# Optimization experiments

Hardware: AMD Instinct MI355X
Metric: run time of the kernel (lower is better)

The kernel has to match this reference:

```python
import jax, jax.numpy as jnp
import numpy as np

NUM_CLASSES = 17
NUM_ENSEMBLE = 10
TAU = 10.0
TOP_K = 20  # min(self.k=20, filter_K=200)
EPS = 1e-12


def _l2norm(x, axis=-1):
    # matches F.normalize: x / max(||x||, 1e-12)
    n = jnp.sqrt(jnp.sum(x * x, axis=axis, keepdims=True))
    return x / jnp.maximum(n, EPS)


def _batch_ensemble(x, weight, alpha_be, gamma_be, ensemble_bias):
    # x: [M, D1] -> [E, M, D2]  (BatchEnsemble.forward, kept in [E, M, D2] layout)
    r = x[None, :, :] * alpha_be[:, None, :]              # [E, M, D1]
    w = jnp.einsum('emd,od->emo', r, weight)              # [E, M, D2]
    return w * gamma_be[:, None, :] + ensemble_bias[:, None, :]


def _compute_logits(z, supports, labels, weight, alpha_be, gamma_be, ensemble_bias):
    mlp_z = _batch_ensemble(z, weight, alpha_be, gamma_be, ensemble_bias)         # [E, B, D2]
    mlp_s = _batch_ensemble(supports, weight, alpha_be, gamma_be, ensemble_bias)  # [E, N, D2]
    lbl = labels / (jnp.sum(labels, axis=0, keepdims=True) + EPS)                 # [N, C]
    centroids = jnp.einsum('nc,end->ecd', lbl, mlp_s)                             # [E, C, D2]
    zn = _l2norm(mlp_z)
    cn = _l2norm(centroids)
    return TAU * jnp.einsum('ebd,ecd->ebc', zn, cn)                               # [E, B, C]


def _cosine_distance(X, Y):
    Xn = _l2norm(X, axis=1)
    Yn = _l2norm(Y, axis=1)
    XX = jnp.sum(Xn * Xn, axis=1)[:, None]   # [B, 1]
    YY = jnp.sum(Yn * Yn, axis=1)            # [N]
    XY = 2.0 * (Xn @ Yn.T)                   # [B, N]
    return XX + YY - XY


def _target_generation(z, supports, labels, weight, alpha_be, gamma_be, ensemble_bias):
    dist = _cosine_distance(z, supports)      # [B, N]
    W = jnp.exp(-dist)
    B = W.shape[0]
    _, idx = jax.lax.top_k(W, TOP_K)                                   # [B, K]
    mask = jnp.zeros_like(W).at[jnp.arange(B)[:, None], idx].set(1.0)  # [B, N]
    temp = _compute_logits(supports, supports, labels, weight, alpha_be, gamma_be, ensemble_bias)  # [E, N, C]
    tgt_oh = jax.nn.one_hot(jnp.argmax(temp, axis=-1), NUM_CLASSES, dtype=temp.dtype)  # [E, N, C]
    soft = jax.nn.softmax(temp, axis=-1)
    targets = jnp.einsum('bn,enc->ebc', mask, tgt_oh)
    targets = targets / (jnp.sum(targets, axis=2, keepdims=True) + EPS)
    outputs = jnp.einsum('bn,enc->ebc', mask, soft)
    outputs = outputs / (jnp.sum(outputs, axis=2, keepdims=True) + EPS)
    outputs = jnp.mean(outputs, axis=0)   # [B, C]
    return targets, outputs


def setup_inputs() -> dict:
    key = jax.random.key(0)
    ks = jax.random.split(key, 7)
    B, N, D1, D2, E, C = 4096, 3400, 2048, 1024, NUM_ENSEMBLE, NUM_CLASSES
    z = jax.random.normal(ks[0], (B, D1), dtype=jnp.float32)
    supports = jax.random.normal(ks[1], (N, D1), dtype=jnp.float32)
    y = jax.random.randint(ks[2], (N,), 0, C)
    labels = jax.nn.one_hot(y, C, dtype=jnp.float32)
    weight = jax.random.normal(ks[3], (D2, D1), dtype=jnp.float32) * 0.02
    alpha_be = 1.0 + 0.1 * jax.random.normal(ks[4], (E, D1), dtype=jnp.float32)
    gamma_be = 1.0 + 0.1 * jax.random.normal(ks[5], (E, D2), dtype=jnp.float32)
    ensemble_bias = jnp.zeros((E, D2), dtype=jnp.float32)
    return {"z": z, "supports": supports, "labels": labels, "weight": weight,
            "alpha_be": alpha_be, "gamma_be": gamma_be, "ensemble_bias": ensemble_bias}


def reference(z, supports, labels, weight, alpha_be, gamma_be, ensemble_bias):
    targets, outputs = _target_generation(z, supports, labels, weight, alpha_be, gamma_be, ensemble_bias)
    logits = _compute_logits(z, supports, labels, weight, alpha_be, gamma_be, ensemble_bias)  # [E, B, C]
    return outputs, logits
```

## Files before the change

### kernel.cpp

```cpp
#include <hip/hip_runtime.h>
#include <math.h>

#define B_    4096
#define N_    3400
#define NP2_  3584
#define D1_   2048
#define D2_   1024
#define E_    10
#define NE_   (E_ * D2_)
#define NDOT_ 256
#define NEX_  (NE_ + NDOT_)
#define ZOFF_ 3456
#define MR_   7680
#define EC_   170
#define C_    17
#define TOPK_ 20
#define CAND_ 24
#define TAU_  10.0f

typedef __bf16 bf16x8 __attribute__((ext_vector_type(8)));
typedef __bf16 bf16x4 __attribute__((ext_vector_type(4)));
typedef float  f32x4  __attribute__((ext_vector_type(4)));

#define MFMA_(a,b,c) __builtin_amdgcn_mfma_f32_16x16x32_bf16(a,b,c,0,0,0)

__device__ inline float wsum64(float v){
  #pragma unroll
  for (int m = 1; m < 64; m <<= 1) v += __shfl_xor(v, m);
  return v;
}

__device__ __forceinline__ void gload_lds16(const unsigned short* g, unsigned short* l){
  __builtin_amdgcn_global_load_lds(
      (const __attribute__((address_space(1))) void*)g,
      (__attribute__((address_space(3))) void*)l, 16, 0, 0);
}

__global__ __launch_bounds__(256)
void prep_rows(const float* __restrict__ X, unsigned short* __restrict__ hi,
               float* __restrict__ rinv){
  const int r = blockIdx.x, t = threadIdx.x;
  const float4* x4 = reinterpret_cast<const float4*>(X + (long)r * D1_);
  bf16x4* h4 = reinterpret_cast<bf16x4*>(hi + (long)r * D1_);
  float ss = 0.f;
  #pragma unroll
  for (int it = 0; it < 2; ++it){
    int i = t + it * 256;
    float4 v = x4[i];
    float f[4] = {v.x, v.y, v.z, v.w};
    bf16x4 h;
    #pragma unroll
    for (int j = 0; j < 4; ++j){
      ss += f[j] * f[j];
      h[j] = (__bf16)f[j];
    }
    h4[i] = h;
  }
  __shared__ float red[256];
  red[t] = ss; __syncthreads();
  for (int s = 128; s; s >>= 1){ if (t < s) red[t] += red[t + s]; __syncthreads(); }
  if (t == 0) rinv[r] = 1.f / fmaxf(sqrtf(red[0]), 1e-12f);
}

__global__ __launch_bounds__(256)
void zfill_all(uint4* p0, long n0, uint4* p1, long n1, uint4* p2, long n2,
               uint4* p3, long n3, uint4* p4, long n4){
  long i = (long)blockIdx.x * 256 + threadIdx.x;
  uint4 zz = make_uint4(0,0,0,0);
  if (i < n0){ p0[i] = zz; return; } i -= n0;
  if (i < n1){ p1[i] = zz; return; } i -= n1;
  if (i < n2){ p2[i] = zz; return; } i -= n2;
  if (i < n3){ p3[i] = zz; return; } i -= n3;
  if (i < n4){ p4[i] = zz; }
}

__global__ __launch_bounds__(256)
void labelprep(const float* __restrict__ labels, int* __restrict__ y, float* __restrict__ cnt){
  int n = blockIdx.x * 256 + threadIdx.x;
  if (n >= N_) return;
  int c = 0;
  #pragma unroll
  for (int cc = 0; cc < C_; ++cc) if (labels[n * C_ + cc] > 0.5f) c = cc;
  y[n] = c;
  atomicAdd(&cnt[c], 1.0f);
}

__global__ __launch_bounds__(256)
void wfold(const float* __restrict__ W, const float* __restrict__ alpha,
           unsigned short* __restrict__ wbf){
  long i = (long)blockIdx.x * 256 + threadIdx.x;
  const long perE = (long)D2_ * D1_ / 4;
  int e = (int)(i / perE);
  long r = i - (long)e * perE;
  int k4 = (int)(r & (D1_/4 - 1));
  float4 wv = reinterpret_cast<const float4*>(W)[r];
  float4 av = reinterpret_cast<const float4*>(alpha + (long)e * D1_)[k4];
  bf16x4 o;
  o[0] = (__bf16)(wv.x * av.x);
  o[1] = (__bf16)(wv.y * av.y);
  o[2] = (__bf16)(wv.z * av.z);
  o[3] = (__bf16)(wv.w * av.w);
  reinterpret_cast<bf16x4*>(wbf)[i] = o;
}

__global__ __launch_bounds__(256)
void transposeW(const float* __restrict__ W, float* __restrict__ WT){
  __shared__ float tile[32][33];
  const int bx = blockIdx.x, by = blockIdx.y;
  const int tx = threadIdx.x & 31, ty = threadIdx.x >> 5;
  #pragma unroll
  for (int i = 0; i < 4; ++i)
    tile[ty + i*8][tx] = W[(long)(by*32 + ty + i*8) * D1_ + bx*32 + tx];
  __syncthreads();
  #pragma unroll
  for (int i = 0; i < 4; ++i)
    WT[(long)(bx*32 + ty + i*8) * D2_ + by*32 + tx] = tile[tx][ty + i*8];
}

__global__ __launch_bounds__(256)
void pbuild(const float* __restrict__ S, const int* __restrict__ y,
            const float* __restrict__ cnt, float* __restrict__ part){
  __shared__ float acc[C_ * 256];
  __shared__ float winv[C_];
  const int t = threadIdx.x, kb = blockIdx.x * 256, s = blockIdx.y;
  #pragma unroll
  for (int c = 0; c < C_; ++c) acc[c * 256 + t] = 0.f;
  if (t < C_) winv[t] = 1.f / (cnt[t] + 1e-12f);
  __syncthreads();
  const int n0 = s * 425, n1 = n0 + 425;
  for (int n = n0; n < n1; ++n){
    int c = y[n];
    acc[c * 256 + t] += winv[c] * S[(long)n * D1_ + kb + t];
  }
  #pragma unroll
  for (int c = 0; c < C_; ++c)
    part[((long)s * C_ + c) * D1_ + kb + t] = acc[c * 256 + t];
}

__global__ __launch_bounds__(256)
void pa2(const float* __restrict__ part, const float* __restrict__ alpha,
         float* __restrict__ A2){
  int i = blockIdx.x * 256 + threadIdx.x;
  if (i >= EC_ * D1_) return;
  int ec = i >> 11, k = i & (D1_ - 1);
  int e = ec / C_, c = ec - e * C_;
  float s = 0.f;
  #pragma unroll
  for (int kz = 0; kz < 8; ++kz) s += part[((long)kz * C_ + c) * D1_ + k];
  A2[i] = s * alpha[(long)e * D1_ + k];
}

__global__ __launch_bounds__(256)
void redcent(const float* __restrict__ part2, const float* __restrict__ gamma,
             const float* __restrict__ bias, const float* __restrict__ cnt,
             float* __restrict__ cent){
  int i = blockIdx.x * 256 + threadIdx.x;
  if (i >= EC_ * D2_) return;
  int ec = i >> 10, d = i & (D2_ - 1);
  int e = ec / C_, c = ec - e * C_;
  float s = 0.f;
  #pragma unroll
  for (int kz = 0; kz < 8; ++kz) s += part2[(long)kz * EC_ * D2_ + i];
  float sc = cnt[c] / (cnt[c] + 1e-12f);
  cent[i] = gamma[(long)e * D2_ + d] * s + bias[(long)e * D2_ + d] * sc;
}

__global__ __launch_bounds__(256)
void normgcn(float* __restrict__ cent, const float* __restrict__ gamma,
             const float* __restrict__ bias, float* __restrict__ gcn,
             float* __restrict__ bconst){
  const int ec = blockIdx.x, t = threadIdx.x;
  const int e = ec / C_;
  float4* c4 = reinterpret_cast<float4*>(cent + (long)ec * D2_);
  float4 v = c4[t];
  float ss = v.x*v.x + v.y*v.y + v.z*v.z + v.w*v.w;
  __shared__ float red[256];
  red[t] = ss; __syncthreads();
  for (int s = 128; s; s >>= 1){ if (t < s) red[t] += red[t + s]; __syncthreads(); }
  float rinv = 1.f / fmaxf(sqrtf(red[0]), 1e-12f);
  v.x *= rinv; v.y *= rinv; v.z *= rinv; v.w *= rinv;
  c4[t] = v;
  float4 g = reinterpret_cast<const float4*>(gamma + (long)e * D2_)[t];
  reinterpret_cast<float4*>(gcn + (long)ec * D2_)[t] =
      make_float4(g.x*v.x, g.y*v.y, g.z*v.z, g.w*v.w);
  float4 bb = reinterpret_cast<const float4*>(bias + (long)e * D2_)[t];
  float bs = bb.x*v.x + bb.y*v.y + bb.z*v.z + bb.w*v.w;
  __syncthreads();
  red[t] = bs; __syncthreads();
  for (int s = 128; s; s >>= 1){ if (t < s) red[t] += red[t + s]; __syncthreads(); }
  if (t == 0) bconst[ec] = red[0];
}

__global__ __launch_bounds__(256)
void redgb(const float* __restrict__ part2, const float* __restrict__ alpha,
           unsigned short* __restrict__ wbf){
  int i = blockIdx.x * 256 + threadIdx.x;
  if (i >= EC_ * D1_) return;
  int ec = i >> 11, k = i & (D1_ - 1);
  int e = ec / C_;
  float s = 0.f;
  #pragma unroll
  for (int kz = 0; kz < 8; ++kz) s += part2[(long)kz * EC_ * D1_ + i];
  __bf16 b = (__bf16)(alpha[(long)e * D1_ + k] * s);
  wbf[(long)(NE_ + ec) * D1_ + k] = *(unsigned short*)&b;
}

__global__ __launch_bounds__(256)
void gemm64k(const float* __restrict__ A, int lda,
             const float* __restrict__ Bm, int ldb,
             float* __restrict__ part, int M, int N, int KC)
{
  __shared__ float As[16][68];
  __shared__ float Bs[16][68];
  const int kz = blockIdx.z;
  const int m0 = blockIdx.y * 64, n0 = blockIdx.x * 64;
  const int t  = threadIdx.x;
  const int lr = t >> 2;
  const int lk = (t & 3) << 2;
  const int ty4 = (t >> 4) << 2;
  const int tx4 = (t & 15) << 2;
  const bool aok = (m0 + lr) < M;
  const bool bok = (n0 + lr) < N;
  const float* ap = A  + (long)(m0 + lr) * lda + lk;
  const float* bp = Bm + (long)(n0 + lr) * ldb + lk;
  float acc[4][4] = {{0.f}};
  const int k0b = kz * KC, k0e = k0b + KC;
  for (int k0 = k0b; k0 < k0e; k0 += 16){
    float4 av = make_float4(0,0,0,0), bv = make_float4(0,0,0,0);
    if (aok) av = *reinterpret_cast<const float4*>(ap + k0);
    if (bok) bv = *reinterpret_cast<const float4*>(bp + k0);
    As[lk+0][lr] = av.x; As[lk+1][lr] = av.y; As[lk+2][lr] = av.z; As[lk+3][lr] = av.w;
    Bs[lk+0][lr] = bv.x; Bs[lk+1][lr] = bv.y; Bs[lk+2][lr] = bv.z; Bs[lk+3][lr] = bv.w;
    __syncthreads();
    #pragma unroll
    for (int kk = 0; kk < 16; ++kk){
      float4 a = *reinterpret_cast<const float4*>(&As[kk][ty4]);
      float4 b = *reinterpret_cast<const float4*>(&Bs[kk][tx4]);
      float aa[4] = {a.x, a.y, a.z, a.w};
      float bb[4] = {b.x, b.y, b.z, b.w};
      #pragma unroll
      for (int i = 0; i < 4; ++i)
        #pragma unroll
        for (int j = 0; j < 4; ++j)
          acc[i][j] += aa[i] * bb[j];
    }
    __syncthreads();
  }
  float* Out = part + (long)kz * M * N;
  #pragma unroll
  for (int i = 0; i < 4; ++i){
    int m = m0 + ty4 + i;
    if (m >= M) continue;
    #pragma unroll
    for (int j = 0; j < 4; ++j){
      int n = n0 + tx4 + j;
      if (n >= N) continue;
      Out[(long)m * N + n] = acc[i][j];
    }
  }
}

#define SA0(buf, kt) { gload_lds16(a0p+(kt)*64, &LA[buf][d00]); gload_lds16(a0p+(kt)*64+32, &LA[buf][d01]); }
#define SA1(buf, kt) { gload_lds16(a1p+(kt)*64, &LA[buf][d10]); gload_lds16(a1p+(kt)*64+32, &LA[buf][d11]); }
#define SB0(buf, kt) { gload_lds16(b0p+(kt)*64, &LB[buf][d00]); gload_lds16(b0p+(kt)*64+32, &LB[buf][d01]); }
#define SB1(buf, kt) { gload_lds16(b1p+(kt)*64, &LB[buf][d10]); gload_lds16(b1p+(kt)*64+32, &LB[buf][d11]); }

#define RD_A03(cb) { _Pragma("unroll") for (int i = 0; i < 4; ++i){ \
    ar[i][0] = *(const bf16x8*)&LA[cb][raB + (unsigned)(i*2  )*512]; \
    ar[i][1] = *(const bf16x8*)&LA[cb][raB + (unsigned)(i*2+1)*512]; } }
#define RD_A47(cb) { _Pragma("unroll") for (int i = 0; i < 4; ++i){ \
    ar[i][0] = *(const bf16x8*)&LA[cb][raB + (unsigned)((4+i)*2  )*512]; \
    ar[i][1] = *(const bf16x8*)&LA[cb][raB + (unsigned)((4+i)*2+1)*512]; } }
#define RD_B01(cb) { _Pragma("unroll") for (int j = 0; j < 2; ++j){ \
    brA[j][0] = *(const bf16x8*)&LB[cb][rbB + (unsigned)(j*2  )*512]; \
    brA[j][1] = *(const bf16x8*)&LB[cb][rbB + (unsigned)(j*2+1)*512]; } }
#define RD_B23(cb) { _Pragma("unroll") for (int j = 0; j < 2; ++j){ \
    brB[j][0] = *(const bf16x8*)&LB[cb][rbB + (unsigned)((2+j)*2  )*512]; \
    brB[j][1] = *(const bf16x8*)&LB[cb][rbB + (unsigned)((2+j)*2+1)*512]; } }

#define MM_Q0 { _Pragma("unroll") for (int ks = 0; ks < 2; ++ks) \
    _Pragma("unroll") for (int i = 0; i < 4; ++i) \
    _Pragma("unroll") for (int j = 0; j < 2; ++j) \
      acc[i][j] = MFMA_(ar[i][ks], brA[j][ks], acc[i][j]); }
#define MM_Q1 { _Pragma("unroll") for (int ks = 0; ks < 2; ++ks) \
    _Pragma("unroll") for (int i = 0; i < 4; ++i) \
    _Pragma("unroll") for (int j = 0; j < 2; ++j) \
      acc[i][2+j] = MFMA_(ar[i][ks], brB[j][ks], acc[i][2+j]); }
#define MM_Q2 { _Pragma("unroll") for (int ks = 0; ks < 2; ++ks) \
    _Pragma("unroll") for (int i = 0; i < 4; ++i) \
    _Pragma("unroll") for (int j = 0; j < 2; ++j) \
      acc[4+i][2+j] = MFMA_(ar[i][ks], brB[j][ks], acc[4+i][2+j]); }
#define MM_Q3 { _Pragma("unroll") for (int ks = 0; ks < 2; ++ks) \
    _Pragma("unroll") for (int i = 0; i < 4; ++i) \
    _Pragma("unroll") for (int j = 0; j < 2; ++j) \
      acc[4+i][j] = MFMA_(ar[i][ks], brA[j][ks], acc[4+i][j]); }

#define PH_TAIL \
  __builtin_amdgcn_s_barrier(); \
  asm volatile("s_waitcnt lgkmcnt(0)" ::: "memory"); \
  __builtin_amdgcn_sched_barrier(0); \
  __builtin_amdgcn_s_setprio(1);
#define PH_END \
  __builtin_amdgcn_s_setprio(0); \
  __builtin_amdgcn_s_barrier();
#define PH_END_W(more) \
  __builtin_amdgcn_s_setprio(0); \
  if (more) asm volatile("s_waitcnt vmcnt(4)" ::: "memory"); \
  else      asm volatile("s_waitcnt vmcnt(0)" ::: "memory"); \
  __builtin_amdgcn_sched_barrier(0); \
  __builtin_amdgcn_s_barrier();

#define K8_LOOP \
  bf16x8 ar[4][2], brA[2][2], brB[2][2]; \
   \
  SA0(0, 0); SA1(0, 0); SB0(0, 0); SB1(0, 0); \
  SB0(1, 1); SB1(1, 1); \
  asm volatile("s_waitcnt vmcnt(4)" ::: "memory"); \
  __builtin_amdgcn_sched_barrier(0); \
  __builtin_amdgcn_s_barrier(); \
  for (int it = 0; it < 16; ++it){ \
    const int kt = it * 2; \
    const bool more = (it < 15); \
     \
    RD_A03(0); RD_B01(0); SA0(1, kt + 1); \
    PH_TAIL; MM_Q0; PH_END; \
     \
    RD_B23(0); SA1(1, kt + 1); \
    PH_TAIL; MM_Q1; PH_END; \
     \
    RD_A47(0); if (more) SB0(0, kt + 2); \
    PH_TAIL; MM_Q2; PH_END; \
     \
    if (more) SB1(0, kt + 2); \
    PH_TAIL; MM_Q3; PH_END_W(more); \
     \
    RD_A03(1); RD_B01(1); if (more) SA0(0, kt + 2); \
    PH_TAIL; MM_Q0; PH_END; \
     \
    RD_B23(1); if (more) SA1(0, kt + 2); \
    PH_TAIL; MM_Q1; PH_END; \
     \
    RD_A47(1); if (more) SB0(1, kt + 3); \
    PH_TAIL; MM_Q2; PH_END; \
     \
    if (more) SB1(1, kt + 3); \
    PH_TAIL; MM_Q3; PH_END_W(more); \
  }

__global__ __launch_bounds__(512)
void sc2(const unsigned short* __restrict__ zh, const unsigned short* __restrict__ sh,
         const float* __restrict__ zinv, const float* __restrict__ sinv,
         float* __restrict__ Out)
{
  __shared__ unsigned short LA[2][16384];
  __shared__ unsigned short LB[2][16384];
  const int n0 = blockIdx.x * 256;
  const int m0 = blockIdx.y * 256;
  const int t = threadIdx.x, lane = t & 63, w = t >> 6;
  const int wm = w >> 2, wn = w & 3;
  const int r15 = lane & 15, kb = lane >> 4;

  const unsigned short* a0p = zh + (long)(m0 +       w*16 + r15) * D1_ + kb*8;
  const unsigned short* a1p = zh + (long)(m0 + 128 + w*16 + r15) * D1_ + kb*8;
  const unsigned short* b0p = sh + (long)(n0 +       w*16 + r15) * D1_ + kb*8;
  const unsigned short* b1p = sh + (long)(n0 + 128 + w*16 + r15) * D1_ + kb*8;
  const unsigned d00 = (unsigned)(w*2)*512,     d01 = (unsigned)(w*2+1)*512;
  const unsigned d10 = (unsigned)((8+w)*2)*512, d11 = (unsigned)((8+w)*2+1)*512;
  const unsigned raB = (unsigned)wm*8192 + (unsigned)lane*8;
  const unsigned rbB = (unsigned)wn*4096 + (unsigned)lane*8;

  f32x4 acc[8][4];
  #pragma unroll
  for (int i = 0; i < 8; ++i)
    #pragma unroll
    for (int j = 0; j < 4; ++j)
      acc[i][j] = (f32x4){0.f, 0.f, 0.f, 0.f};

  K8_LOOP

  const int mb = m0 + wm * 128 + kb * 4;
  const int nc0 = n0 + wn * 64 + r15;
  #pragma unroll
  for (int j = 0; j < 4; ++j){
    int n = nc0 + j * 16;
    if (n >= N_) continue;
    float si = sinv[n];
    #pragma unroll
    for (int i = 0; i < 8; ++i)
      #pragma unroll
      for (int r = 0; r < 4; ++r){
        int m = mb + i*16 + r;
        Out[(long)m * N_ + n] = acc[i][j][r] * zinv[m] * si;
      }
  }
}

__global__ __launch_bounds__(512)
void nd2(const unsigned short* __restrict__ A,
         const unsigned short* __restrict__ Bw,
         const float* __restrict__ gamma,
         const float* __restrict__ bias,
         float* __restrict__ norm2,
         float* __restrict__ dots)
{
  __shared__ unsigned short LA[2][16384];
  __shared__ unsigned short LB[2][16384];
  const int n0 = blockIdx.x * 256;
  const int m0 = blockIdx.y * 256;
  const int t = threadIdx.x, lane = t & 63, w = t >> 6;
  const int wm = w >> 2, wn = w & 3;
  const int r15 = lane & 15, kb = lane >> 4;

  const unsigned short* a0p = A  + (long)(m0 +       w*16 + r15) * D1_ + kb*8;
  const unsigned short* a1p = A  + (long)(m0 + 128 + w*16 + r15) * D1_ + kb*8;
  const unsigned short* b0p = Bw + (long)(n0 +       w*16 + r15) * D1_ + kb*8;
  const unsigned short* b1p = Bw + (long)(n0 + 128 + w*16 + r15) * D1_ + kb*8;
  const unsigned d00 = (unsigned)(w*2)*512,     d01 = (unsigned)(w*2+1)*512;
  const unsigned d10 = (unsigned)((8+w)*2)*512, d11 = (unsigned)((8+w)*2+1)*512;
  const unsigned raB = (unsigned)wm*8192 + (unsigned)lane*8;
  const unsigned rbB = (unsigned)wn*4096 + (unsigned)lane*8;

  f32x4 acc[8][4];
  #pragma unroll
  for (int i = 0; i < 8; ++i)
    #pragma unroll
    for (int j = 0; j < 4; ++j)
      acc[i][j] = (f32x4){0.f, 0.f, 0.f, 0.f};

  K8_LOOP

  if (n0 < NE_){
    const int e = n0 >> 10;
    float g4[4], b4[4];
    #pragma unroll
    for (int j = 0; j < 4; ++j){
      int n = n0 + wn * 64 + j * 16 + r15;
      g4[j] = gamma[n]; b4[j] = bias[n];
    }
    float rs[32];
    #pragma unroll
    for (int i = 0; i < 8; ++i)
      #pragma unroll
      for (int r = 0; r < 4; ++r){
        float s = 0.f;
        #pragma unroll
        for (int j = 0; j < 4; ++j){
          float v = acc[i][j][r] * g4[j] + b4[j];
          s += v * v;
        }
        rs[i*4 + r] = s;
      }
    #pragma unroll
    for (int msk = 1; msk < 16; msk <<= 1)
      #pragma unroll
      for (int q = 0; q < 32; ++q) rs[q] += __shfl_xor(rs[q], msk);
    float* red = (float*)&LA[0][0];
    if (r15 == 0){
      #pragma unroll
      for (int i = 0; i < 8; ++i)
        #pragma unroll
        for (int r = 0; r < 4; ++r)
          red[w * 128 + i*16 + kb*4 + r] = rs[i*4 + r];
    }
    __syncthreads();
    if (t < 256){
      int wmg = t >> 7;
      float v = 0.f;
      #pragma unroll
      for (int q = 0; q < 4; ++q)
        v += red[(wmg*4 + q) * 128 + (t & 127)];
      atomicAdd(&norm2[(long)(m0 + t) * E_ + e], v);
    }
  } else {
    const int dc0 = n0 - NE_ + wn * 64 + r15;
    const int mb = m0 + wm * 128 + kb * 4;
    #pragma unroll
    for (int j = 0; j < 4; ++j){
      int dc = dc0 + j * 16;
      #pragma unroll
      for (int i = 0; i < 8; ++i)
        #pragma unroll
        for (int r = 0; r < 4; ++r)
          dots[(long)(mb + i*16 + r) * NDOT_ + dc] = acc[i][j][r];
    }
  }
}

__global__ __launch_bounds__(256)
void topk_rescore(const float* __restrict__ scores, const float* __restrict__ z,
                  const float* __restrict__ S, const float* __restrict__ sinv,
                  int* __restrict__ idx){
  const int b = blockIdx.x, t = threadIdx.x;
  const int l = t & 63, wid = t >> 6;
  const float* row = scores + (long)b * N_;
  float v[14];
  #pragma unroll
  for (int j = 0; j < 14; ++j){
    int i = t + j * 256;
    v[j] = (i < N_) ? row[i] : -3.0e38f;
  }
  __shared__ float wv4[4];
  __shared__ int   wi4[4];
  __shared__ int   cand[CAND_];
  __shared__ float sval[CAND_];
  for (int it = 0; it < CAND_; ++it){
    float bv = -3.0e38f; int bj = 0;
    #pragma unroll
    for (int j = 0; j < 14; ++j)
      if (v[j] > bv){ bv = v[j]; bj = j; }
    int bi = t + bj * 256;
    #pragma unroll
    for (int m = 1; m < 64; m <<= 1){
      float ov = __shfl_xor(bv, m);
      int   oi = __shfl_xor(bi, m);
      if (ov > bv || (ov == bv && oi < bi)){ bv = ov; bi = oi; }
    }
    if (l == 0){ wv4[wid] = bv; wi4[wid] = bi; }
    __syncthreads();
    float gv = wv4[0]; int gi = wi4[0];
    #pragma unroll
    for (int k = 1; k < 4; ++k){
      float ov = wv4[k]; int oi = wi4[k];
      if (ov > gv || (ov == gv && oi < gi)){ gv = ov; gi = oi; }
    }
    if (t == 0) cand[it] = gi;
    const int ot = gi & 255, oj = gi >> 8;
    #pragma unroll
    for (int j = 0; j < 14; ++j)
      if (t == ot && j == oj) v[j] = -3.0e38f;
    __syncthreads();
  }
  const float4* zr = reinterpret_cast<const float4*>(z + (long)b * D1_);
  for (int ci = wid; ci < CAND_; ci += 4){
    int n = cand[ci];
    const float4* sr = reinterpret_cast<const float4*>(S + (long)n * D1_);
    float p = 0.f;
    #pragma unroll
    for (int j = 0; j < 8; ++j){
      float4 a = zr[l + j * 64];
      float4 c = sr[l + j * 64];
      p += a.x*c.x + a.y*c.y + a.z*c.z + a.w*c.w;
    }
    p = wsum64(p);
    if (l == 0) sval[ci] = p * sinv[n];
  }
  __syncthreads();
  if (t < 64){
    float vv = (l < CAND_) ? sval[l] : -3.0e38f;
    int   nn = (l < CAND_) ? cand[l] : 0x7fffffff;
    for (int it = 0; it < TOPK_; ++it){
      float bv = vv; int bi = nn, bl = l;
      #pragma unroll
      for (int m = 1; m < 64; m <<= 1){
        float ov = __shfl_xor(bv, m);
        int   oi = __shfl_xor(bi, m);
        int   ol = __shfl_xor(bl, m);
        if (ov > bv || (ov == bv && oi < bi)){ bv = ov; bi = oi; bl = ol; }
      }
      if (l == 0) idx[b * TOPK_ + it] = bi;
      if (l == bl) vv = -3.0e38f;
    }
  }
}

__global__ __launch_bounds__(256)
void soft_build(const float* __restrict__ dots, const float* __restrict__ norm2,
                const float* __restrict__ bconst, float* __restrict__ soft){
  int id = blockIdx.x * 256 + threadIdx.x;
  if (id >= N_ * E_) return;
  int e = id % E_, n = id / E_;
  float rinv = 1.f / fmaxf(sqrtf(norm2[(long)n * E_ + e]), 1e-12f);
  float tv[C_];
  #pragma unroll
  for (int c = 0; c < C_; ++c)
    tv[c] = TAU_ * (dots[(long)n * NDOT_ + e*C_ + c] + bconst[e*C_ + c]) * rinv;
  float m = tv[0];
  #pragma unroll
  for (int c = 1; c < C_; ++c) m = fmaxf(m, tv[c]);
  float p[C_]; float sum = 0.f;
  #pragma unroll
  for (int c = 0; c < C_; ++c){ p[c] = expf(tv[c] - m); sum += p[c]; }
  float is = 1.f / sum;
  #pragma unroll
  for (int c = 0; c < C_; ++c)
    soft[((long)e * N_ + n) * C_ + c] = p[c] * is;
}

__global__ __launch_bounds__(256)
void logits_fin(const float* __restrict__ dots, const float* __restrict__ norm2,
                const float* __restrict__ bconst, float* __restrict__ out){
  int id = blockIdx.x * 256 + threadIdx.x;
  if (id >= B_ * E_) return;
  int e = id % E_, b = id / E_;
  int m = ZOFF_ + b;
  float rinv = 1.f / fmaxf(sqrtf(norm2[(long)m * E_ + e]), 1e-12f);
  float* op = out + (size_t)B_ * C_ + ((long)e * B_ + b) * C_;
  #pragma unroll
  for (int c = 0; c < C_; ++c)
    op[c] = TAU_ * (dots[(long)m * NDOT_ + e*C_ + c] + bconst[e*C_ + c]) * rinv;
}

__global__ __launch_bounds__(256)
void outputs_k(const float* __restrict__ soft, const int* __restrict__ idx, float* __restrict__ out){
  const int lane = threadIdx.x & 63;
  const int b = blockIdx.x * 4 + (threadIdx.x >> 6);
  const int* id = idx + b * TOPK_;
  float o = 0.f;
  for (int e = 0; e < E_; ++e){
    float S = 0.f;
    const float* se = soft + (long)e * N_ * C_;
    #pragma unroll
    for (int k = 0; k < TOPK_; ++k){
      int n = id[k];
      if (lane < C_) S += se[(long)n * C_ + lane];
    }
    float tot = wsum64(S);
    o += S / (tot + 1e-12f);
  }
  if (lane < C_) out[(long)b * C_ + lane] = o * (1.f / E_);
}

extern "C" void kernel_launch(void* const* d_in, const int* in_sizes, int n_in,
                              void* d_out, int out_size, void* d_ws, size_t ws_size,
                              hipStream_t stream){
  const float* z        = (const float*)d_in[0];
  const float* supports = (const float*)d_in[1];
  const float* labels   = (const float*)d_in[2];
  const float* weight   = (const float*)d_in[3];
  const float* alpha    = (const float*)d_in[4];
  const float* gamma    = (const float*)d_in[5];
  const float* bias     = (const float*)d_in[6];
  float* out = (float*)d_out;

  char* w = (char*)d_ws;
  size_t off = 0;
  auto alloc = [&](size_t bytes)->char*{
    char* p = w + off;
    off = (off + bytes + 255) & ~(size_t)255;
    return p;
  };

  float* zinv = (float*)alloc((size_t)B_ * 4);
  float* sinv = (float*)alloc((size_t)N_ * 4);
  float* cnt  = (float*)alloc((size_t)C_ * 4);
  int*   y    = (int*)  alloc((size_t)N_ * 4);
  int*   idx  = (int*)  alloc((size_t)B_ * TOPK_ * 4);
  unsigned short* SZ  = (unsigned short*)alloc((size_t)MR_ * D1_ * 2);
  unsigned short* wbf = (unsigned short*)alloc((size_t)NEX_ * D1_ * 2);
  float* WT     = (float*)alloc((size_t)D1_ * D2_ * 4);
  float* part   = (float*)alloc((size_t)8 * C_ * D1_ * 4);
  float* A2     = (float*)alloc((size_t)EC_ * D1_ * 4);
  float* cent   = (float*)alloc((size_t)EC_ * D2_ * 4);
  float* gcn    = (float*)alloc((size_t)EC_ * D2_ * 4);
  float* bconst = (float*)alloc((size_t)256 * 4);
  float* scores = (float*)alloc((size_t)B_ * N_ * 4);
  float* dots   = (float*)alloc((size_t)MR_ * NDOT_ * 4);
  float* norm2  = (float*)alloc((size_t)MR_ * E_ * 4);
  float* soft   = (float*)alloc((size_t)E_ * N_ * C_ * 4);
  float* part2  = (float*)alloc((size_t)8 * EC_ * D1_ * 4);
  (void)ws_size; (void)in_sizes; (void)n_in; (void)out_size;

  unsigned short* sh = SZ;
  unsigned short* zh = SZ + (size_t)ZOFF_ * D1_;

  {
    long n0 = 14336, n1 = 32768, n2 = 22016, n3 = 19200, n4 = 5;
    long tot = n0 + n1 + n2 + n3 + n4;
    zfill_all<<<(int)((tot + 255) / 256), 256, 0, stream>>>(
        (uint4*)(sh + (size_t)N_ * D1_), n0,
        (uint4*)(SZ + (size_t)(ZOFF_ + B_) * D1_), n1,
        (uint4*)(wbf + (size_t)(NE_ + EC_) * D1_), n2,
        (uint4*)norm2, n3,
        (uint4*)cnt, n4);
  }
  labelprep<<<(N_ + 255) / 256, 256, 0, stream>>>(labels, y, cnt);

  prep_rows<<<B_, 256, 0, stream>>>(z, zh, zinv);
  prep_rows<<<N_, 256, 0, stream>>>(supports, sh, sinv);
  wfold<<<(int)((long)NE_ * D1_ / 4 / 256), 256, 0, stream>>>(weight, alpha, wbf);
  transposeW<<<dim3(D1_ / 32, D2_ / 32), 256, 0, stream>>>(weight, WT);

  sc2<<<dim3(NP2_ / 256, B_ / 256, 1), 512, 0, stream>>>(
      zh, sh, zinv, sinv, scores);
  topk_rescore<<<B_, 256, 0, stream>>>(scores, z, supports, sinv, idx);

  pbuild<<<dim3(D1_ / 256, 8), 256, 0, stream>>>(supports, y, cnt, part);
  pa2<<<(EC_ * D1_ + 255) / 256, 256, 0, stream>>>(part, alpha, A2);
  gemm64k<<<dim3(D2_ / 64, 3, 8), 256, 0, stream>>>(
      A2, D1_, weight, D1_, part2, EC_, D2_, 256);
  redcent<<<(EC_ * D2_ + 255) / 256, 256, 0, stream>>>(part2, gamma, bias, cnt, cent);
  normgcn<<<EC_, 256, 0, stream>>>(cent, gamma, bias, gcn, bconst);
  gemm64k<<<dim3(D1_ / 64, 3, 8), 256, 0, stream>>>(
      gcn, D2_, WT, D2_, part2, EC_, D1_, 128);
  redgb<<<(EC_ * D1_ + 255) / 256, 256, 0, stream>>>(part2, alpha, wbf);

  nd2<<<dim3(NEX_ / 256, MR_ / 256, 1), 512, 0, stream>>>(
      SZ, wbf, gamma, bias, norm2, dots);

  soft_build<<<(N_ * E_ + 255) / 256, 256, 0, stream>>>(dots, norm2, bconst, soft);
  outputs_k<<<B_ / 4, 256, 0, stream>>>(soft, idx, out);
  logits_fin<<<(B_ * E_ + 255) / 256, 256, 0, stream>>>(dots, norm2, bconst, out);
}
```

Before: 897.9 us.

## Swizzle GEMM workgroups across XCDs and drop per-iteration barriers in top-k

```diff
diff --git a/kernel.cpp b/kernel.cpp
--- a/kernel.cpp
+++ b/kernel.cpp
@@ -312,7 +312,6 @@
 
 #define K8_LOOP \
   bf16x8 ar[4][2], brA[2][2], brB[2][2]; \
-   \
   SA0(0, 0); SA1(0, 0); SB0(0, 0); SB1(0, 0); \
   SB0(1, 1); SB1(1, 1); \
   asm volatile("s_waitcnt vmcnt(4)" ::: "memory"); \
@@ -321,31 +320,31 @@
   for (int it = 0; it < 16; ++it){ \
     const int kt = it * 2; \
     const bool more = (it < 15); \
-     \
     RD_A03(0); RD_B01(0); SA0(1, kt + 1); \
     PH_TAIL; MM_Q0; PH_END; \
-     \
     RD_B23(0); SA1(1, kt + 1); \
     PH_TAIL; MM_Q1; PH_END; \
-     \
     RD_A47(0); if (more) SB0(0, kt + 2); \
     PH_TAIL; MM_Q2; PH_END; \
-     \
     if (more) SB1(0, kt + 2); \
     PH_TAIL; MM_Q3; PH_END_W(more); \
-     \
     RD_A03(1); RD_B01(1); if (more) SA0(0, kt + 2); \
     PH_TAIL; MM_Q0; PH_END; \
-     \
     RD_B23(1); if (more) SA1(0, kt + 2); \
     PH_TAIL; MM_Q1; PH_END; \
-     \
     RD_A47(1); if (more) SB0(1, kt + 3); \
     PH_TAIL; MM_Q2; PH_END; \
-     \
     if (more) SB1(1, kt + 3); \
     PH_TAIL; MM_Q3; PH_END_W(more); \
   }
+
+#define XCD_SWZ(wgid_out) \
+  const int gx_ = gridDim.x; \
+  const int nwg_ = gx_ * gridDim.y; \
+  int bidf_ = blockIdx.y * gx_ + blockIdx.x; \
+  const int q_ = nwg_ >> 3, r_ = nwg_ & 7; \
+  int xcd_ = bidf_ & 7, pos_ = bidf_ >> 3; \
+  int wgid_out = (xcd_ < r_ ? xcd_ * (q_ + 1) : r_ * (q_ + 1) + (xcd_ - r_) * q_) + pos_;
 
 __global__ __launch_bounds__(512)
 void sc2(const unsigned short* __restrict__ zh, const unsigned short* __restrict__ sh,
@@ -354,8 +353,9 @@
 {
   __shared__ unsigned short LA[2][16384];
   __shared__ unsigned short LB[2][16384];
-  const int n0 = blockIdx.x * 256;
-  const int m0 = blockIdx.y * 256;
+  XCD_SWZ(wgid)
+  const int n0 = (wgid % gx_) * 256;
+  const int m0 = (wgid / gx_) * 256;
   const int t = threadIdx.x, lane = t & 63, w = t >> 6;
   const int wm = w >> 2, wn = w & 3;
   const int r15 = lane & 15, kb = lane >> 4;
@@ -405,8 +405,9 @@
 {
   __shared__ unsigned short LA[2][16384];
   __shared__ unsigned short LB[2][16384];
-  const int n0 = blockIdx.x * 256;
-  const int m0 = blockIdx.y * 256;
+  XCD_SWZ(wgid)
+  const int n0 = (wgid % gx_) * 256;
+  const int m0 = (wgid / gx_) * 256;
   const int t = threadIdx.x, lane = t & 63, w = t >> 6;
   const int wm = w >> 2, wn = w & 3;
   const int r15 = lane & 15, kb = lane >> 4;
@@ -499,8 +500,8 @@
     int i = t + j * 256;
     v[j] = (i < N_) ? row[i] : -3.0e38f;
   }
-  __shared__ float wv4[4];
-  __shared__ int   wi4[4];
+  __shared__ float wval[4 * CAND_];
+  __shared__ int   widx[4 * CAND_];
   __shared__ int   cand[CAND_];
   __shared__ float sval[CAND_];
   for (int it = 0; it < CAND_; ++it){
@@ -515,21 +516,35 @@
       int   oi = __shfl_xor(bi, m);
       if (ov > bv || (ov == bv && oi < bi)){ bv = ov; bi = oi; }
     }
-    if (l == 0){ wv4[wid] = bv; wi4[wid] = bi; }
-    __syncthreads();
-    float gv = wv4[0]; int gi = wi4[0];
-    #pragma unroll
-    for (int k = 1; k < 4; ++k){
-      float ov = wv4[k]; int oi = wi4[k];
-      if (ov > gv || (ov == gv && oi < gi)){ gv = ov; gi = oi; }
-    }
-    if (t == 0) cand[it] = gi;
-    const int ot = gi & 255, oj = gi >> 8;
+    if (l == 0){ wval[wid * CAND_ + it] = bv; widx[wid * CAND_ + it] = bi; }
+    const int ot = bi & 255, oj = bi >> 8;
     #pragma unroll
     for (int j = 0; j < 14; ++j)
       if (t == ot && j == oj) v[j] = -3.0e38f;
-    __syncthreads();
-  }
+  }
+  __syncthreads();
+  if (wid == 0){
+    float m0v = wval[l];
+    int   m0i = widx[l];
+    float m1v = (l < 32) ? wval[64 + l] : -3.0e38f;
+    int   m1i = (l < 32) ? widx[64 + l] : 0x7fffffff;
+    for (int it = 0; it < CAND_; ++it){
+      float bv = m0v; int bi = m0i; int sel = 0;
+      if (m1v > bv || (m1v == bv && m1i < bi)){ bv = m1v; bi = m1i; sel = 1; }
+      int bl = l;
+      #pragma unroll
+      for (int m = 1; m < 64; m <<= 1){
+        float ov = __shfl_xor(bv, m);
+        int   oi = __shfl_xor(bi, m);
+        int   ol = __shfl_xor(bl, m);
+        int   os = __shfl_xor(sel, m);
+        if (ov > bv || (ov == bv && oi < bi)){ bv = ov; bi = oi; bl = ol; sel = os; }
+      }
+      if (l == 0) cand[it] = bi;
+      if (l == bl){ if (sel) m1v = -3.0e38f; else m0v = -3.0e38f; }
+    }
+  }
+  __syncthreads();
   const float4* zr = reinterpret_cast<const float4*>(z + (long)b * D1_);
   for (int ci = wid; ci < CAND_; ci += 4){
     int n = cand[ci];
```

Result: no change. 915.6 us (+2.0%).
